# Kernel tuning notes

Measured on AMD Instinct MI355X. Metric: run time of the kernel, lower is better.

Reference implementation:

```python
import jax, jax.numpy as jnp
import numpy as np

H = 1024


def setup_inputs() -> dict:
    key = jax.random.key(0)
    ks = jax.random.split(key, 8)
    B, S = 32, 2048
    query = jax.random.normal(ks[0], (B, 1, H), dtype=jnp.float32)
    keys = jax.random.normal(ks[1], (B, S, H), dtype=jnp.float32)
    s = 1.0 / np.sqrt(H)
    Wa_w = jax.random.uniform(ks[2], (H, H), jnp.float32, -s, s)
    Wa_b = jax.random.uniform(ks[3], (H,), jnp.float32, -s, s)
    Ua_w = jax.random.uniform(ks[4], (H, H), jnp.float32, -s, s)
    Ua_b = jax.random.uniform(ks[5], (H,), jnp.float32, -s, s)
    Va_w = jax.random.uniform(ks[6], (1, H), jnp.float32, -s, s)
    Va_b = jax.random.uniform(ks[7], (1,), jnp.float32, -s, s)
    return {"query": query, "keys": keys, "Wa_w": Wa_w, "Wa_b": Wa_b,
            "Ua_w": Ua_w, "Ua_b": Ua_b, "Va_w": Va_w, "Va_b": Va_b}


def reference(query, keys, Wa_w, Wa_b, Ua_w, Ua_b, Va_w, Va_b):
    # query: [B,1,H]; keys: [B,S,H]
    q_proj = jnp.einsum('boh,kh->bok', query, Wa_w) + Wa_b      # [B,1,H], broadcasts over S
    k_proj = jnp.einsum('bsh,kh->bsk', keys, Ua_w) + Ua_b       # [B,S,H]
    e = jnp.tanh(q_proj + k_proj)                               # [B,S,H]
    scores = jnp.einsum('bsh,h->bs', e, Va_w[0]) + Va_b[0]      # [B,S]
    weights = jax.nn.softmax(scores, axis=1)[:, None, :]        # [B,1,S]
    context = jnp.einsum('bos,bsh->boh', weights, keys)         # [B,1,H]
    return (context, weights)
```

## Files before the change

kernel.cpp:

```cpp
#include <hip/hip_runtime.h>
#include <hip/hip_bf16.h>

#define H 1024
#define B 32
#define S 2048

typedef __attribute__((ext_vector_type(8))) short bf16x8;
typedef __attribute__((ext_vector_type(4))) float f32x4;

union U4 { uint4 u; bf16x8 b; };

__device__ __forceinline__ unsigned short f2bf(float f) {
    unsigned u = __float_as_uint(f);
    unsigned r = (u + 0x7fffu + ((u >> 16) & 1u)) >> 16;
    return (unsigned short)r;
}

__device__ __forceinline__ uint4 pack8(float4 x, float4 y) {
    uint4 p;
    p.x = (unsigned)f2bf(x.x) | ((unsigned)f2bf(x.y) << 16);
    p.y = (unsigned)f2bf(x.z) | ((unsigned)f2bf(x.w) << 16);
    p.z = (unsigned)f2bf(y.x) | ((unsigned)f2bf(y.y) << 16);
    p.w = (unsigned)f2bf(y.z) | ((unsigned)f2bf(y.w) << 16);
    return p;
}

__device__ __forceinline__ float ftanh(float x) {
    float x2 = __builtin_amdgcn_fmed3f(x + x, -30.f, 30.f);
    float e = __expf(x2);
    return 1.f - 2.f * __builtin_amdgcn_rcpf(e + 1.f);
}

__device__ __forceinline__ void async_copy16(const void* g, void* l) {
    __builtin_amdgcn_global_load_lds(
        (const __attribute__((address_space(1))) unsigned int*)g,
        (__attribute__((address_space(3))) unsigned int*)l, 16, 0, 0);
}

__global__ void k0_swizzle(const float* __restrict__ Ua, uint4* __restrict__ UaSw) {
    int t = blockIdx.x * 256 + threadIdx.x;
    int lane = t & 63;
    int nt = (t >> 6) & 7;
    int kc = (t >> 9) & 31;
    int nb = t >> 14;
    int n = nb * 128 + nt * 16 + (lane & 15);
    int k = kc * 32 + ((lane >> 4) & 3) * 8;
    const float4* src = (const float4*)(Ua + (size_t)n * H + k);
    UaSw[t] = pack8(src[0], src[1]);
}

__global__ void k1_qproj(const float* __restrict__ q, const float* __restrict__ Wa,
                         const float* __restrict__ Wab, const float* __restrict__ Uab,
                         float* __restrict__ qp) {
    int b = blockIdx.y;
    int n = blockIdx.x * 256 + threadIdx.x;
    __shared__ float qs[H];
    for (int i = threadIdx.x; i < H; i += 256) qs[i] = q[b * H + i];
    __syncthreads();
    float acc = 0.f;
    const float4* wr = (const float4*)(Wa + (size_t)n * H);
#pragma unroll 4
    for (int h4 = 0; h4 < H / 4; h4++) {
        float4 w = wr[h4];
        acc += qs[h4 * 4 + 0] * w.x + qs[h4 * 4 + 1] * w.y +
               qs[h4 * 4 + 2] * w.z + qs[h4 * 4 + 3] * w.w;
    }
    qp[b * H + n] = acc + Wab[n] + Uab[n];
}

__global__ __launch_bounds__(256, 3) void k2_scores(
    const float* __restrict__ keys, const uint4* __restrict__ UaSw,
    const float* __restrict__ qp, const float* __restrict__ Vaw,
    float* __restrict__ scores) {
    __shared__ uint4 As[512];
    __shared__ uint4 Bs[512];
    __shared__ float part[2][128];

    const int tid = threadIdx.x;
    const int lane = tid & 63;
    const int wave = tid >> 6;
    const int wm = wave >> 1, wn = wave & 1;
    const int nb = blockIdx.x;
    const int mb = blockIdx.y;
    const int b = mb >> 4;
    const int s0 = (mb & 15) << 7;

    const int el = tid & 63;
    const int srow0 = s0 + (tid >> 6) * 16 + (el & 15);
    const int srow1 = srow0 + 64;
    const int kofs = ((el >> 4) & 3) * 8;
    const float4* ka0 = (const float4*)(keys + ((size_t)b * S + srow0) * H + kofs);
    const float4* ka1 = (const float4*)(keys + ((size_t)b * S + srow1) * H + kofs);
    const uint4* srcB = UaSw + (size_t)nb * 32 * 512;

    f32x4 acc[4][4];
#pragma unroll
    for (int mt = 0; mt < 4; mt++)
#pragma unroll
        for (int nt = 0; nt < 4; nt++) acc[mt][nt] = (f32x4){0.f, 0.f, 0.f, 0.f};

    float4 x0 = ka0[0], y0 = ka0[1], x1 = ka1[0], y1 = ka1[1];

    for (int kc = 0; kc < 32; kc++) {
        __syncthreads();
        async_copy16(srcB + (size_t)kc * 512 + tid,       &Bs[tid]);
        async_copy16(srcB + (size_t)kc * 512 + tid + 256, &Bs[tid + 256]);
        As[tid]       = pack8(x0, y0);
        As[tid + 256] = pack8(x1, y1);
        if (kc < 31) {
            x0 = ka0[(kc + 1) * 8]; y0 = ka0[(kc + 1) * 8 + 1];
            x1 = ka1[(kc + 1) * 8]; y1 = ka1[(kc + 1) * 8 + 1];
        }
        __syncthreads();
        U4 af[4], bf[4];
#pragma unroll
        for (int mt = 0; mt < 4; mt++) af[mt].u = As[(wm * 4 + mt) * 64 + lane];
#pragma unroll
        for (int nt = 0; nt < 4; nt++) bf[nt].u = Bs[(wn * 4 + nt) * 64 + lane];
#pragma unroll
        for (int mt = 0; mt < 4; mt++)
#pragma unroll
            for (int nt = 0; nt < 4; nt++)
                acc[mt][nt] = __builtin_amdgcn_mfma_f32_16x16x32_bf16(
                    af[mt].b, bf[nt].b, acc[mt][nt], 0, 0, 0);
    }

    const int col = lane & 15, q = lane >> 4;
    float qv[4], vv[4];
#pragma unroll
    for (int nt = 0; nt < 4; nt++) {
        int n = nb * 128 + (wn * 4 + nt) * 16 + col;
        qv[nt] = qp[b * H + n];
        vv[nt] = Vaw[n];
    }
#pragma unroll
    for (int mt = 0; mt < 4; mt++) {
        float rs[4] = {0.f, 0.f, 0.f, 0.f};
#pragma unroll
        for (int nt = 0; nt < 4; nt++)
#pragma unroll
            for (int r = 0; r < 4; r++)
                rs[r] += ftanh(acc[mt][nt][r] + qv[nt]) * vv[nt];
#pragma unroll
        for (int r = 0; r < 4; r++) {
            float v = rs[r];
            v += __shfl_xor(v, 1, 64);
            v += __shfl_xor(v, 2, 64);
            v += __shfl_xor(v, 4, 64);
            v += __shfl_xor(v, 8, 64);
            if (col == 0) part[wn][wm * 64 + mt * 16 + q * 4 + r] = v;
        }
    }
    __syncthreads();
    if (tid < 128)
        atomicAdd(&scores[b * S + s0 + tid], part[0][tid] + part[1][tid]);
}

__global__ void k3_softmax(const float* __restrict__ scores, float* __restrict__ out) {
    int b = blockIdx.x, t = threadIdx.x;
    __shared__ float red[256];
    float v[8];
    float lm = -1e30f;
#pragma unroll
    for (int i = 0; i < 8; i++) {
        v[i] = scores[b * S + i * 256 + t];
        lm = fmaxf(lm, v[i]);
    }
    red[t] = lm;
    __syncthreads();
    for (int s = 128; s > 0; s >>= 1) {
        if (t < s) red[t] = fmaxf(red[t], red[t + s]);
        __syncthreads();
    }
    float m = red[0];
    __syncthreads();
    float ls = 0.f;
#pragma unroll
    for (int i = 0; i < 8; i++) {
        v[i] = __expf(v[i] - m);
        ls += v[i];
    }
    red[t] = ls;
    __syncthreads();
    for (int s = 128; s > 0; s >>= 1) {
        if (t < s) red[t] += red[t + s];
        __syncthreads();
    }
    float inv = 1.f / red[0];
#pragma unroll
    for (int i = 0; i < 8; i++) out[B * H + b * S + i * 256 + t] = v[i] * inv;
}

__global__ __launch_bounds__(256) void k4_ctx(const float* __restrict__ keys,
                                              const float* __restrict__ out_w,
                                              float* __restrict__ out_c) {
    int sc = blockIdx.x, b = blockIdx.y;
    int t = threadIdx.x;
    __shared__ float wl[256];
    wl[t] = out_w[B * H + b * S + sc * 256 + t];
    __syncthreads();
    const float4* kp = (const float4*)(keys + ((size_t)b * S + sc * 256) * H) + t;
    float4 acc = {0.f, 0.f, 0.f, 0.f};
#pragma unroll 8
    for (int s = 0; s < 256; s++) {
        float4 kv = kp[(size_t)s * 256];
        float w = wl[s];
        acc.x += w * kv.x; acc.y += w * kv.y;
        acc.z += w * kv.z; acc.w += w * kv.w;
    }
    float* dst = out_c + b * H + t * 4;
    atomicAdd(dst + 0, acc.x);
    atomicAdd(dst + 1, acc.y);
    atomicAdd(dst + 2, acc.z);
    atomicAdd(dst + 3, acc.w);
}

extern "C" void kernel_launch(void* const* d_in, const int* in_sizes, int n_in,
                              void* d_out, int out_size, void* d_ws, size_t ws_size,
                              hipStream_t stream) {
    const float* query = (const float*)d_in[0];
    const float* keys  = (const float*)d_in[1];
    const float* Wa_w  = (const float*)d_in[2];
    const float* Wa_b  = (const float*)d_in[3];
    const float* Ua_w  = (const float*)d_in[4];
    const float* Ua_b  = (const float*)d_in[5];
    const float* Va_w  = (const float*)d_in[6];
    float* out = (float*)d_out;

    uint4* UaSw = (uint4*)d_ws;
    float* qp = (float*)((char*)d_ws + (2u << 20));
    float* scores = (float*)((char*)d_ws + (2u << 20) + (128u << 10));

    hipMemsetAsync(d_out, 0, B * H * sizeof(float), stream);
    hipMemsetAsync(scores, 0, B * S * sizeof(float), stream);

    k0_swizzle<<<512, 256, 0, stream>>>(Ua_w, UaSw);
    k1_qproj<<<dim3(4, B), 256, 0, stream>>>(query, Wa_w, Wa_b, Ua_b, qp);
    k2_scores<<<dim3(8, 512), 256, 0, stream>>>(keys, UaSw, qp, Va_w, scores);
    k3_softmax<<<B, 256, 0, stream>>>(scores, out);
    k4_ctx<<<dim3(S / 256, B), 256, 0, stream>>>(keys, out, out);
}
```

Before: 668.3 us.

## Fuse softmax into context kernel and remap score-GEMM block order for L2 reuse

```diff
diff --git a/kernel.cpp b/kernel.cpp
--- a/kernel.cpp
+++ b/kernel.cpp
@@ -80,8 +80,11 @@
     const int lane = tid & 63;
     const int wave = tid >> 6;
     const int wm = wave >> 1, wn = wave & 1;
-    const int nb = blockIdx.x;
-    const int mb = blockIdx.y;
+    const int lid = blockIdx.x;
+    const int c = lid & 7;
+    const int qq = lid >> 3;
+    const int nb = qq & 7;
+    const int mb = (qq >> 3) * 8 + c;
     const int b = mb >> 4;
     const int s0 = (mb & 15) << 7;
 
@@ -125,7 +128,7 @@
                     af[mt].b, bf[nt].b, acc[mt][nt], 0, 0, 0);
     }
 
-    const int col = lane & 15, q = lane >> 4;
+    const int col = lane & 15, qd = lane >> 4;
     float qv[4], vv[4];
 #pragma unroll
     for (int nt = 0; nt < 4; nt++) {
@@ -148,7 +151,7 @@
             v += __shfl_xor(v, 2, 64);
             v += __shfl_xor(v, 4, 64);
             v += __shfl_xor(v, 8, 64);
-            if (col == 0) part[wn][wm * 64 + mt * 16 + q * 4 + r] = v;
+            if (col == 0) part[wn][wm * 64 + mt * 16 + qd * 4 + r] = v;
         }
     }
     __syncthreads();
@@ -156,9 +159,14 @@
         atomicAdd(&scores[b * S + s0 + tid], part[0][tid] + part[1][tid]);
 }
 
-__global__ void k3_softmax(const float* __restrict__ scores, float* __restrict__ out) {
-    int b = blockIdx.x, t = threadIdx.x;
+__global__ __launch_bounds__(256) void k4_ctx(const float* __restrict__ keys,
+                                              const float* __restrict__ scores,
+                                              float* __restrict__ out) {
+    int sc = blockIdx.x, b = blockIdx.y;
+    int t = threadIdx.x;
     __shared__ float red[256];
+    __shared__ float wl[128];
+
     float v[8];
     float lm = -1e30f;
 #pragma unroll
@@ -176,10 +184,7 @@
     __syncthreads();
     float ls = 0.f;
 #pragma unroll
-    for (int i = 0; i < 8; i++) {
-        v[i] = __expf(v[i] - m);
-        ls += v[i];
-    }
+    for (int i = 0; i < 8; i++) ls += __expf(v[i] - m);
     red[t] = ls;
     __syncthreads();
     for (int s = 128; s > 0; s >>= 1) {
@@ -187,28 +192,24 @@
         __syncthreads();
     }
     float inv = 1.f / red[0];
-#pragma unroll
-    for (int i = 0; i < 8; i++) out[B * H + b * S + i * 256 + t] = v[i] * inv;
-}
-
-__global__ __launch_bounds__(256) void k4_ctx(const float* __restrict__ keys,
-                                              const float* __restrict__ out_w,
-                                              float* __restrict__ out_c) {
-    int sc = blockIdx.x, b = blockIdx.y;
-    int t = threadIdx.x;
-    __shared__ float wl[256];
-    wl[t] = out_w[B * H + b * S + sc * 256 + t];
-    __syncthreads();
-    const float4* kp = (const float4*)(keys + ((size_t)b * S + sc * 256) * H) + t;
+
+    if (t < 128) {
+        float w = __expf(scores[b * S + sc * 128 + t] - m) * inv;
+        wl[t] = w;
+        out[B * H + b * S + sc * 128 + t] = w;
+    }
+    __syncthreads();
+
+    const float4* kp = (const float4*)(keys + ((size_t)b * S + sc * 128) * H) + t;
     float4 acc = {0.f, 0.f, 0.f, 0.f};
 #pragma unroll 8
-    for (int s = 0; s < 256; s++) {
+    for (int s = 0; s < 128; s++) {
         float4 kv = kp[(size_t)s * 256];
         float w = wl[s];
         acc.x += w * kv.x; acc.y += w * kv.y;
         acc.z += w * kv.z; acc.w += w * kv.w;
     }
-    float* dst = out_c + b * H + t * 4;
+    float* dst = out + b * H + t * 4;
     atomicAdd(dst + 0, acc.x);
     atomicAdd(dst + 1, acc.y);
     atomicAdd(dst + 2, acc.z);
@@ -236,7 +237,6 @@
 
     k0_swizzle<<<512, 256, 0, stream>>>(Ua_w, UaSw);
     k1_qproj<<<dim3(4, B), 256, 0, stream>>>(query, Wa_w, Wa_b, Ua_b, qp);
-    k2_scores<<<dim3(8, 512), 256, 0, stream>>>(keys, UaSw, qp, Va_w, scores);
-    k3_softmax<<<B, 256, 0, stream>>>(scores, out);
-    k4_ctx<<<dim3(S / 256, B), 256, 0, stream>>>(keys, out, out);
-}
+    k2_scores<<<4096, 256, 0, stream>>>(keys, UaSw, qp, Va_w, scores);
+    k4_ctx<<<dim3(16, B), 256, 0, stream>>>(keys, scores, out);
+}
```

Result: no change. 658.2 us (-1.5%).
